# Performance work log

Measured on AMD Instinct MI355X. Metric: run time of the kernel, lower is better.

The kernel has to match this reference:

```python
import jax, jax.numpy as jnp
import numpy as np

ALPHA = 0.2  # LeakyReLU negative slope
NEG_INF = -1e9


def setup_inputs() -> dict:
    key = jax.random.key(0)
    k1, k2, k3, k4 = jax.random.split(key, 4)
    B, N, F_in, F_out = 4, 4096, 128, 128
    h = jax.random.normal(k1, (B, N, F_in), dtype=jnp.float32)
    adj = jax.random.randint(k2, (B, N, N), 0, 2, dtype=jnp.int32)
    # Xavier-uniform init matching nn.Linear weights
    limW = np.sqrt(6.0 / (F_in + F_out))
    W = jax.random.uniform(k3, (F_in, F_out), jnp.float32, -limW, limW)
    lima = np.sqrt(6.0 / (2 * F_out + 1))
    a = jax.random.uniform(k4, (2 * F_out,), jnp.float32, -lima, lima)
    return {"h": h, "adj": adj, "W": W, "a": a}


def reference(h, adj, W, a):
    # h: (B, N, F_in), adj: (B, N, N) int, W: (F_in, F_out), a: (2*F_out,)
    F_out = W.shape[1]
    Wh = jnp.einsum("bnf,fo->bno", h, W)  # (B, N, F_out)
    a_i, a_j = a[:F_out], a[F_out:]
    # e_ij = leakyrelu(a . [Wh_i, Wh_j]) = leakyrelu(a_i.Wh_i + a_j.Wh_j)
    si = Wh @ a_i  # (B, N) contribution of destination node i
    sj = Wh @ a_j  # (B, N) contribution of source node j
    e = si[:, :, None] + sj[:, None, :]  # (B, N, N)
    e = jnp.where(e > 0, e, ALPHA * e)  # LeakyReLU
    e = jnp.where(adj > 0, e, NEG_INF)  # masked scores
    attention = jax.nn.softmax(e, axis=-1)  # (B, N, N)
    # dropout is identity in eval mode
    h_prime = jnp.einsum("bij,bjo->bio", attention, Wh)  # (B, N, F_out)
    return jax.nn.elu(h_prime)  # concat=True -> ELU
```

## Files before the change

kernel.cpp:

```cpp
#include <hip/hip_runtime.h>

#define GN 4096
#define GF 128
#define GB 4

typedef __attribute__((ext_vector_type(8))) short short8;
typedef __attribute__((ext_vector_type(4))) float floatx4;

static __device__ __forceinline__ unsigned short f2bf(float x){
  unsigned int u = __float_as_uint(x);
  u += 0x7FFFu + ((u >> 16) & 1u);
  return (unsigned short)(u >> 16);
}

__global__ __launch_bounds__(256)
void gat_prep(const float* __restrict__ h, const float* __restrict__ W,
              const float* __restrict__ a, unsigned short* __restrict__ whB,
              float* __restrict__ si_g, unsigned short* __restrict__ EFh)
{
  __shared__ float hl[16*GF];
  __shared__ float red[2][2][16];
  const int tid = threadIdx.x;
  const int b   = blockIdx.x >> 8;
  const int r0  = (blockIdx.x & 255) << 4;
  const int o = tid & 127, g = tid >> 7;

  const float4* hb4 = (const float4*)(h + ((size_t)(b*GN + r0))*GF);
  ((float4*)hl)[tid]       = hb4[tid];
  ((float4*)hl)[tid + 256] = hb4[tid + 256];
  __syncthreads();

  float acc[8];
  #pragma unroll
  for (int r=0;r<8;++r) acc[r] = 0.f;
  const float* Wp = W + o;
  for (int f4=0; f4<32; ++f4){
    const float w0 = Wp[(f4*4+0)*GF];
    const float w1 = Wp[(f4*4+1)*GF];
    const float w2 = Wp[(f4*4+2)*GF];
    const float w3 = Wp[(f4*4+3)*GF];
    #pragma unroll
    for (int r=0;r<8;++r){
      const float4 h4 = *(const float4*)&hl[((g<<3)+r)*GF + (f4<<2)];
      acc[r] = fmaf(h4.x, w0, acc[r]);
      acc[r] = fmaf(h4.y, w1, acc[r]);
      acc[r] = fmaf(h4.z, w2, acc[r]);
      acc[r] = fmaf(h4.w, w3, acc[r]);
    }
  }

  const float ai = a[o], aj = a[GF + o];
  const int lane = tid & 63, wh = (tid >> 6) & 1;
  #pragma unroll
  for (int r=0;r<8;++r){
    float vi = acc[r]*ai, vj = acc[r]*aj;
    #pragma unroll
    for (int off=32; off; off>>=1){ vi += __shfl_down(vi, off); vj += __shfl_down(vj, off); }
    if (lane == 0){ red[0][wh][(g<<3)+r] = vi; red[1][wh][(g<<3)+r] = vj; }
  }

  unsigned short us[8] __attribute__((aligned(16)));
  #pragma unroll
  for (int r=0;r<8;++r) us[r] = f2bf(acc[r]);
  {
    const int j0 = r0 + (g<<3);
    unsigned short* dst = whB + (((size_t)(b*128 + (j0>>5))*128 + o)<<5) + (j0&31);
    *(uint4*)dst = *(const uint4*)us;
  }

  __syncthreads();
  if (tid < 16){
    si_g[b*GN + r0 + tid] = red[0][0][tid] + red[0][1][tid];
  } else if (tid < 32){
    const int r = tid - 16;
    const float vsj = red[1][0][r] + red[1][1][r];
    EFh[(size_t)b*8192 + r0 + r]        = f2bf(__expf(vsj));
    EFh[(size_t)b*8192 + 4096 + r0 + r] = f2bf(__expf(0.2f*vsj));
  }
}

__global__ __launch_bounds__(256, 2)
void gat_main(const int* __restrict__ adj, const unsigned short* __restrict__ whB,
              const float* __restrict__ si_g, const unsigned short* __restrict__ EFh,
              float* __restrict__ out)
{
  __shared__ __align__(16) char smem[(64*129 + 64)*4];
  unsigned short* sEj = (unsigned short*)smem;
  unsigned int*   bitsW  = (unsigned int*)(smem + 16384);
  unsigned long long* bits64 = (unsigned long long*)(smem + 16384);
  float* smemc = (float*)smem;

  const int tid  = threadIdx.x;
  const int wave = tid >> 6, lane = tid & 63;
  const int b  = (blockIdx.x >> 1) & 3;
  const int i0 = ((((blockIdx.x >> 3) << 1) | (blockIdx.x & 1))) << 4;
  const int m = lane & 15, quad = lane >> 4, q8 = quad << 3;

  const int jw = wave << 10, jw32 = wave << 5;

  {
    const uint4* Eg = (const uint4*)(EFh + (size_t)b*8192);
    uint4* sE4 = (uint4*)sEj;
    #pragma unroll
    for (int k=0;k<4;++k) sE4[tid + (k<<8)] = Eg[tid + (k<<8)];
  }

  {
    const int* adjb = adj + ((size_t)(b*GN + i0))*GN + jw;
    #pragma unroll 2
    for (int r = 0; r < 16; ++r){
      const int* src = adjb + (size_t)r*GN;
      int v[16];
      #pragma unroll
      for (int c = 0; c < 16; ++c)
        v[c] = __builtin_nontemporal_load(src + (c<<6) + lane);
      #pragma unroll
      for (int c = 0; c < 16; ++c){
        const unsigned long long mm = __ballot(v[c] > 0);
        if (lane == 0) bits64[r*66 + (wave<<4) + c] = mm;
      }
    }
  }
  __syncthreads();

  const float si_m = si_g[(size_t)b*GN + i0 + m];
  const float Ti = __expf(-si_m);
  const float Ri = __expf(-0.8f*si_m);
  const unsigned short* lanebase = whB + ((size_t)b<<19) + (m<<5) + q8;

  floatx4 acc[8];
  #pragma unroll
  for (int c=0;c<8;++c) acc[c] = (floatx4){0.f,0.f,0.f,0.f};
  floatx4 lfrag = (floatx4){0.f,0.f,0.f,0.f};
  const short8 ones8 = {0x3F80,0x3F80,0x3F80,0x3F80,0x3F80,0x3F80,0x3F80,0x3F80};

  short8 Bcur[8], Bnxt[8];
  #pragma unroll
  for (int c=0;c<8;++c) Bcur[c] = *(const short8*)(lanebase + ((size_t)(jw32+0)<<12) + (c<<9));

  #pragma unroll 4
  for (int it = 0; it < 32; ++it){
    if (it < 31){
      const unsigned short* wn = lanebase + ((size_t)(jw32+it+1)<<12);
      #pragma unroll
      for (int c=0;c<8;++c) Bnxt[c] = *(const short8*)(wn + (c<<9));
    }
    const unsigned int sh = bitsW[m*132 + jw32 + it] >> q8;
    const int jj = jw + (it << 5) + q8;
    const short8 Es = *(const short8*)&sEj[jj];
    const short8 Fs = *(const short8*)&sEj[4096 + jj];
    const unsigned int* Eu = (const unsigned int*)&Es;
    const unsigned int* Fu = (const unsigned int*)&Fs;
    unsigned int aw[4];
    #pragma unroll
    for (int p=0;p<4;++p){
      unsigned int e0 = Eu[p] << 16, e1 = Eu[p] & 0xFFFF0000u;
      unsigned int f0 = Fu[p] << 16, f1 = Fu[p] & 0xFFFF0000u;
      float E0 = __uint_as_float(e0), E1 = __uint_as_float(e1);
      float t0 = Ri*__uint_as_float(f0), t1 = Ri*__uint_as_float(f1);
      float p0 = (E0 > Ti) ? E0 : t0;
      float p1 = (E1 > Ti) ? E1 : t1;
      unsigned int k0 = (unsigned int)(((int)(sh << (31-(2*p))))   >> 31);
      unsigned int k1 = (unsigned int)(((int)(sh << (31-(2*p+1)))) >> 31);
      unsigned int b0 = __float_as_uint(p0) & k0;
      unsigned int b1 = __float_as_uint(p1) & k1;
      aw[p] = ((b0 + 0x8000u) >> 16) | ((b1 + 0x8000u) & 0xFFFF0000u);
    }
    const short8 af = *(const short8*)aw;
    #pragma unroll
    for (int c=0;c<8;++c)
      acc[c] = __builtin_amdgcn_mfma_f32_16x16x32_bf16(af, Bcur[c], acc[c], 0, 0, 0);
    lfrag = __builtin_amdgcn_mfma_f32_16x16x32_bf16(af, ones8, lfrag, 0, 0, 0);
    #pragma unroll
    for (int c=0;c<8;++c) Bcur[c] = Bnxt[c];
  }

  __syncthreads();
  #pragma unroll
  for (int c=0;c<8;++c){
    #pragma unroll
    for (int r=0;r<4;++r){
      smemc[(wave*16 + quad*4 + r)*129 + c*16 + m] = acc[c][r];
    }
  }
  if (m == 0){
    #pragma unroll
    for (int r=0;r<4;++r) smemc[8256 + wave*16 + quad*4 + r] = lfrag[r];
  }
  __syncthreads();

  #pragma unroll
  for (int k=0;k<8;++k){
    const int idx = tid + (k<<8);
    const int row = idx >> 7, col = idx & 127;
    const float s = smemc[row*129+col] + smemc[(16+row)*129+col]
                  + smemc[(32+row)*129+col] + smemc[(48+row)*129+col];
    const float l = smemc[8256+row] + smemc[8256+16+row]
                  + smemc[8256+32+row] + smemc[8256+48+row];
    float v = s / l;
    v = v > 0.f ? v : expm1f(v);
    out[((size_t)(b*GN + i0 + row))*GF + col] = v;
  }
}

extern "C" void kernel_launch(void* const* d_in, const int* in_sizes, int n_in,
                              void* d_out, int out_size, void* d_ws, size_t ws_size,
                              hipStream_t stream)
{
  (void)in_sizes; (void)n_in; (void)out_size; (void)ws_size;
  const float* h   = (const float*)d_in[0];
  const int*   adj = (const int*)d_in[1];
  const float* W   = (const float*)d_in[2];
  const float* a   = (const float*)d_in[3];
  float* out = (float*)d_out;

  char* ws = (char*)d_ws;
  unsigned short* whB   = (unsigned short*)ws;
  float*          si    = (float*)(ws + (size_t)4*1024*1024);
  unsigned short* EFh   = (unsigned short*)(ws + (size_t)4*1024*1024 + 64*1024);

  gat_prep<<<GB*GN/16, 256, 0, stream>>>(h, W, a, whB, si, EFh);
  gat_main<<<GB*GN/16, 256, 0, stream>>>(adj, whB, si, EFh, out);
}
```

Measured before the change: 446.5 us.

## Split adjacency bit-packing into a separate streaming kernel before the main kernel

Moves the conversion of the int32 adjacency matrix into bitmasks out of the attention kernel into a dedicated pack kernel, which writes a compact bit array to the workspace. The main kernel then loads the 16x4096 bit tile directly into shared memory instead of streaming and ballot-packing 256 KB of adj per block. The aim is to turn the adj read into a simple, fully parallel memory-bound pass and shorten the prologue of the MFMA kernel. The cost is an extra launch, extra global write and read of the bit array, and loss of overlap between adj loading and compute within one kernel.

```diff
diff --git a/kernel.cpp b/kernel.cpp
--- a/kernel.cpp
+++ b/kernel.cpp
@@ -11,6 +11,21 @@
   unsigned int u = __float_as_uint(x);
   u += 0x7FFFu + ((u >> 16) & 1u);
   return (unsigned short)(u >> 16);
+}
+
+__global__ __launch_bounds__(256)
+void gat_pack(const int* __restrict__ adj, unsigned int* __restrict__ bits)
+{
+  const int lane = threadIdx.x & 63, wave = threadIdx.x >> 6;
+  const size_t row = (size_t)blockIdx.x * 4 + wave;
+  const int* src = adj + row * GN;
+  unsigned long long* dst = (unsigned long long*)(bits + row * (GN/32));
+  #pragma unroll 8
+  for (int it = 0; it < GN/64; ++it){
+    const int v = src[(it<<6) + lane];
+    const unsigned long long m = __ballot(v > 0);
+    if (lane == 0) dst[it] = m;
+  }
 }
 
 __global__ __launch_bounds__(256)
@@ -80,14 +95,13 @@
 }
 
 __global__ __launch_bounds__(256, 2)
-void gat_main(const int* __restrict__ adj, const unsigned short* __restrict__ whB,
+void gat_main(const unsigned int* __restrict__ adjbits, const unsigned short* __restrict__ whB,
               const float* __restrict__ si_g, const unsigned short* __restrict__ EFh,
               float* __restrict__ out)
 {
   __shared__ __align__(16) char smem[(64*129 + 64)*4];
   unsigned short* sEj = (unsigned short*)smem;
   unsigned int*   bitsW  = (unsigned int*)(smem + 16384);
-  unsigned long long* bits64 = (unsigned long long*)(smem + 16384);
   float* smemc = (float*)smem;
 
   const int tid  = threadIdx.x;
@@ -103,22 +117,12 @@
     uint4* sE4 = (uint4*)sEj;
     #pragma unroll
     for (int k=0;k<4;++k) sE4[tid + (k<<8)] = Eg[tid + (k<<8)];
-  }
-
-  {
-    const int* adjb = adj + ((size_t)(b*GN + i0))*GN + jw;
-    #pragma unroll 2
-    for (int r = 0; r < 16; ++r){
-      const int* src = adjb + (size_t)r*GN;
-      int v[16];
-      #pragma unroll
-      for (int c = 0; c < 16; ++c)
-        v[c] = __builtin_nontemporal_load(src + (c<<6) + lane);
-      #pragma unroll
-      for (int c = 0; c < 16; ++c){
-        const unsigned long long mm = __ballot(v[c] > 0);
-        if (lane == 0) bits64[r*66 + (wave<<4) + c] = mm;
-      }
+    const unsigned int* bg = adjbits + ((size_t)(b*GN + i0))*(GN/32);
+    #pragma unroll
+    for (int k=0;k<8;++k){
+      const int idx = tid + (k<<8);
+      const int row = idx >> 7, w = idx & 127;
+      bitsW[row*132 + w] = bg[(size_t)row*(GN/32) + w];
     }
   }
   __syncthreads();
@@ -218,7 +222,9 @@
   unsigned short* whB   = (unsigned short*)ws;
   float*          si    = (float*)(ws + (size_t)4*1024*1024);
   unsigned short* EFh   = (unsigned short*)(ws + (size_t)4*1024*1024 + 64*1024);
-
+  unsigned int*   bits  = (unsigned int*)(ws + (size_t)4*1024*1024 + 128*1024);
+
+  gat_pack<<<(GB*GN)/4, 256, 0, stream>>>(adj, bits);
   gat_prep<<<GB*GN/16, 256, 0, stream>>>(h, W, a, whB, si, EFh);
-  gat_main<<<GB*GN/16, 256, 0, stream>>>(adj, whB, si, EFh, out);
-}
+  gat_main<<<GB*GN/16, 256, 0, stream>>>(bits, whB, si, EFh, out);
+}
```

After: 472.9 us. +5.9%, slower.

## Process 32 destination rows per block to reuse Wh fragments across two MFMA tiles

Applied to the files above, without the earlier changes.

Each block of gat_main now handles 32 rows instead of 16, so every B fragment of Wh read from global memory feeds two MFMA accumulator sets, halving whB traffic per output row. The explicit double-buffered prefetch of B fragments is dropped in favour of direct loads per iteration, and the bitmask stride changes to 134/67 for the larger tile. The cost is roughly doubled accumulator registers, which may reduce occupancy or cause spills, and half as many blocks in the grid.

```diff
diff --git a/kernel.cpp b/kernel.cpp
--- a/kernel.cpp
+++ b/kernel.cpp
@@ -84,7 +84,7 @@
               const float* __restrict__ si_g, const unsigned short* __restrict__ EFh,
               float* __restrict__ out)
 {
-  __shared__ __align__(16) char smem[(64*129 + 64)*4];
+  __shared__ __align__(16) char smem[16384 + 32*134*4];
   unsigned short* sEj = (unsigned short*)smem;
   unsigned int*   bitsW  = (unsigned int*)(smem + 16384);
   unsigned long long* bits64 = (unsigned long long*)(smem + 16384);
@@ -93,7 +93,7 @@
   const int tid  = threadIdx.x;
   const int wave = tid >> 6, lane = tid & 63;
   const int b  = (blockIdx.x >> 1) & 3;
-  const int i0 = ((((blockIdx.x >> 3) << 1) | (blockIdx.x & 1))) << 4;
+  const int i0 = ((((blockIdx.x >> 3) << 1) | (blockIdx.x & 1))) << 5;
   const int m = lane & 15, quad = lane >> 4, q8 = quad << 3;
 
   const int jw = wave << 10, jw32 = wave << 5;
@@ -108,7 +108,7 @@
   {
     const int* adjb = adj + ((size_t)(b*GN + i0))*GN + jw;
     #pragma unroll 2
-    for (int r = 0; r < 16; ++r){
+    for (int r = 0; r < 32; ++r){
       const int* src = adjb + (size_t)r*GN;
       int v[16];
       #pragma unroll
@@ -117,89 +117,99 @@
       #pragma unroll
       for (int c = 0; c < 16; ++c){
         const unsigned long long mm = __ballot(v[c] > 0);
-        if (lane == 0) bits64[r*66 + (wave<<4) + c] = mm;
+        if (lane == 0) bits64[r*67 + (wave<<4) + c] = mm;
       }
     }
   }
   __syncthreads();
 
-  const float si_m = si_g[(size_t)b*GN + i0 + m];
-  const float Ti = __expf(-si_m);
-  const float Ri = __expf(-0.8f*si_m);
+  const float si0 = si_g[(size_t)b*GN + i0 + m];
+  const float si1 = si_g[(size_t)b*GN + i0 + 16 + m];
+  const float Ti0 = __expf(-si0),      Ti1 = __expf(-si1);
+  const float Ri0 = __expf(-0.8f*si0), Ri1 = __expf(-0.8f*si1);
   const unsigned short* lanebase = whB + ((size_t)b<<19) + (m<<5) + q8;
 
-  floatx4 acc[8];
-  #pragma unroll
-  for (int c=0;c<8;++c) acc[c] = (floatx4){0.f,0.f,0.f,0.f};
-  floatx4 lfrag = (floatx4){0.f,0.f,0.f,0.f};
+  floatx4 acc0[8], acc1[8];
+  #pragma unroll
+  for (int c=0;c<8;++c){ acc0[c] = (floatx4){0.f,0.f,0.f,0.f}; acc1[c] = (floatx4){0.f,0.f,0.f,0.f}; }
+  floatx4 lf0 = (floatx4){0.f,0.f,0.f,0.f}, lf1 = (floatx4){0.f,0.f,0.f,0.f};
   const short8 ones8 = {0x3F80,0x3F80,0x3F80,0x3F80,0x3F80,0x3F80,0x3F80,0x3F80};
 
-  short8 Bcur[8], Bnxt[8];
-  #pragma unroll
-  for (int c=0;c<8;++c) Bcur[c] = *(const short8*)(lanebase + ((size_t)(jw32+0)<<12) + (c<<9));
-
-  #pragma unroll 4
+#define MKAF(dst_, sh_, Ti_, Ri_) do { \
+    unsigned int aw[4]; \
+    _Pragma("unroll") \
+    for (int p=0;p<4;++p){ \
+      unsigned int e0 = Eu[p] << 16, e1 = Eu[p] & 0xFFFF0000u; \
+      unsigned int f0 = Fu[p] << 16, f1 = Fu[p] & 0xFFFF0000u; \
+      float E0 = __uint_as_float(e0), E1 = __uint_as_float(e1); \
+      float t0 = (Ri_)*__uint_as_float(f0), t1 = (Ri_)*__uint_as_float(f1); \
+      float p0 = (E0 > (Ti_)) ? E0 : t0; \
+      float p1 = (E1 > (Ti_)) ? E1 : t1; \
+      unsigned int k0 = (unsigned int)(((int)((sh_) << (31-(2*p))))   >> 31); \
+      unsigned int k1 = (unsigned int)(((int)((sh_) << (31-(2*p+1)))) >> 31); \
+      unsigned int b0 = __float_as_uint(p0) & k0; \
+      unsigned int b1 = __float_as_uint(p1) & k1; \
+      aw[p] = ((b0 + 0x8000u) >> 16) | ((b1 + 0x8000u) & 0xFFFF0000u); \
+    } \
+    dst_ = *(const short8*)aw; \
+  } while(0)
+
+  #pragma unroll 2
   for (int it = 0; it < 32; ++it){
-    if (it < 31){
-      const unsigned short* wn = lanebase + ((size_t)(jw32+it+1)<<12);
-      #pragma unroll
-      for (int c=0;c<8;++c) Bnxt[c] = *(const short8*)(wn + (c<<9));
-    }
-    const unsigned int sh = bitsW[m*132 + jw32 + it] >> q8;
+    const unsigned short* wb = lanebase + ((size_t)(jw32+it)<<12);
+    short8 Bc[8];
+    #pragma unroll
+    for (int c=0;c<8;++c) Bc[c] = *(const short8*)(wb + (c<<9));
+
+    const unsigned int sh0 = bitsW[m*134 + jw32 + it] >> q8;
+    const unsigned int sh1 = bitsW[(m+16)*134 + jw32 + it] >> q8;
     const int jj = jw + (it << 5) + q8;
     const short8 Es = *(const short8*)&sEj[jj];
     const short8 Fs = *(const short8*)&sEj[4096 + jj];
     const unsigned int* Eu = (const unsigned int*)&Es;
     const unsigned int* Fu = (const unsigned int*)&Fs;
-    unsigned int aw[4];
-    #pragma unroll
-    for (int p=0;p<4;++p){
-      unsigned int e0 = Eu[p] << 16, e1 = Eu[p] & 0xFFFF0000u;
-      unsigned int f0 = Fu[p] << 16, f1 = Fu[p] & 0xFFFF0000u;
-      float E0 = __uint_as_float(e0), E1 = __uint_as_float(e1);
-      float t0 = Ri*__uint_as_float(f0), t1 = Ri*__uint_as_float(f1);
-      float p0 = (E0 > Ti) ? E0 : t0;
-      float p1 = (E1 > Ti) ? E1 : t1;
-      unsigned int k0 = (unsigned int)(((int)(sh << (31-(2*p))))   >> 31);
-      unsigned int k1 = (unsigned int)(((int)(sh << (31-(2*p+1)))) >> 31);
-      unsigned int b0 = __float_as_uint(p0) & k0;
-      unsigned int b1 = __float_as_uint(p1) & k1;
-      aw[p] = ((b0 + 0x8000u) >> 16) | ((b1 + 0x8000u) & 0xFFFF0000u);
-    }
-    const short8 af = *(const short8*)aw;
-    #pragma unroll
-    for (int c=0;c<8;++c)
-      acc[c] = __builtin_amdgcn_mfma_f32_16x16x32_bf16(af, Bcur[c], acc[c], 0, 0, 0);
-    lfrag = __builtin_amdgcn_mfma_f32_16x16x32_bf16(af, ones8, lfrag, 0, 0, 0);
-    #pragma unroll
-    for (int c=0;c<8;++c) Bcur[c] = Bnxt[c];
-  }
-
-  __syncthreads();
-  #pragma unroll
-  for (int c=0;c<8;++c){
-    #pragma unroll
-    for (int r=0;r<4;++r){
-      smemc[(wave*16 + quad*4 + r)*129 + c*16 + m] = acc[c][r];
-    }
-  }
-  if (m == 0){
-    #pragma unroll
-    for (int r=0;r<4;++r) smemc[8256 + wave*16 + quad*4 + r] = lfrag[r];
-  }
-  __syncthreads();
-
-  #pragma unroll
-  for (int k=0;k<8;++k){
-    const int idx = tid + (k<<8);
-    const int row = idx >> 7, col = idx & 127;
-    const float s = smemc[row*129+col] + smemc[(16+row)*129+col]
-                  + smemc[(32+row)*129+col] + smemc[(48+row)*129+col];
-    const float l = smemc[8256+row] + smemc[8256+16+row]
-                  + smemc[8256+32+row] + smemc[8256+48+row];
-    float v = s / l;
-    v = v > 0.f ? v : expm1f(v);
-    out[((size_t)(b*GN + i0 + row))*GF + col] = v;
+    short8 af0, af1;
+    MKAF(af0, sh0, Ti0, Ri0);
+    MKAF(af1, sh1, Ti1, Ri1);
+    #pragma unroll
+    for (int c=0;c<8;++c){
+      acc0[c] = __builtin_amdgcn_mfma_f32_16x16x32_bf16(af0, Bc[c], acc0[c], 0, 0, 0);
+      acc1[c] = __builtin_amdgcn_mfma_f32_16x16x32_bf16(af1, Bc[c], acc1[c], 0, 0, 0);
+    }
+    lf0 = __builtin_amdgcn_mfma_f32_16x16x32_bf16(af0, ones8, lf0, 0, 0, 0);
+    lf1 = __builtin_amdgcn_mfma_f32_16x16x32_bf16(af1, ones8, lf1, 0, 0, 0);
+  }
+#undef MKAF
+
+  #pragma unroll 1
+  for (int g = 0; g < 2; ++g){
+    __syncthreads();
+    #pragma unroll
+    for (int c=0;c<8;++c){
+      #pragma unroll
+      for (int r=0;r<4;++r){
+        const float v = g ? acc1[c][r] : acc0[c][r];
+        smemc[(wave*16 + quad*4 + r)*129 + c*16 + m] = v;
+      }
+    }
+    if (m == 0){
+      #pragma unroll
+      for (int r=0;r<4;++r) smemc[8256 + wave*16 + quad*4 + r] = g ? lf1[r] : lf0[r];
+    }
+    __syncthreads();
+
+    #pragma unroll
+    for (int k=0;k<8;++k){
+      const int idx = tid + (k<<8);
+      const int row = idx >> 7, col = idx & 127;
+      const float s = smemc[row*129+col] + smemc[(16+row)*129+col]
+                    + smemc[(32+row)*129+col] + smemc[(48+row)*129+col];
+      const float l = smemc[8256+row] + smemc[8256+16+row]
+                    + smemc[8256+32+row] + smemc[8256+48+row];
+      float v = s / l;
+      v = v > 0.f ? v : expm1f(v);
+      out[((size_t)(b*GN + i0 + (g<<4) + row))*GF + col] = v;
+    }
   }
 }
 
@@ -220,5 +230,5 @@
   unsigned short* EFh   = (unsigned short*)(ws + (size_t)4*1024*1024 + 64*1024);
 
   gat_prep<<<GB*GN/16, 256, 0, stream>>>(h, W, a, whB, si, EFh);
-  gat_main<<<GB*GN/16, 256, 0, stream>>>(adj, whB, si, EFh, out);
-}
+  gat_main<<<GB*GN/32, 256, 0, stream>>>(adj, whB, si, EFh, out);
+}
```

Result: faster. 407.9 us (-8.6%).
